# Optimization experiments

Hardware: AMD Instinct MI355X
Metric: run time of the kernel (lower is better)

Reference implementation:

```python
import jax, jax.numpy as jnp
import numpy as np

B, L, HID = 2, 2048, 4096
NH, NKV, HD = 16, 4, 64
BLOCK = 16
THETA = 8000000.0
EPS = 1e-6
NEG = jnp.finfo(jnp.float32).min


def _rope_tables(theta, L, hd):
    inv_freq = 1.0 / (theta ** (np.arange(0, hd, 2, dtype=np.float32) / hd))  # [hd/2]
    t = np.arange(L, dtype=np.float32)
    freqs = np.outer(t, inv_freq)                      # [L, hd/2]
    emb = np.concatenate([freqs, freqs], axis=-1)      # [L, hd]
    return jnp.asarray(np.cos(emb)), jnp.asarray(np.sin(emb))


def setup_inputs() -> dict:
    key = jax.random.key(0)
    k1, k2, k3 = jax.random.split(key, 3)
    hidden_states = jax.random.normal(k1, (B, L, HID), dtype=jnp.float32)
    Wqkv = jax.random.normal(k2, (HID, (NH + 2 * NKV) * HD), dtype=jnp.float32) * 0.006
    Wo = jax.random.normal(k3, (NH * HD, HID), dtype=jnp.float32) * 0.006
    q_norm_w = jnp.ones((HD,), dtype=jnp.float32)
    k_norm_w = jnp.ones((HD,), dtype=jnp.float32)
    # block-diagonal causal additive mask [1,1,L,L]
    idx = jnp.arange(L)
    same_block = (idx[:, None] // BLOCK) == (idx[None, :] // BLOCK)
    causal = idx[:, None] >= idx[None, :]
    attention_mask = jnp.where(same_block & causal, 0.0, NEG)[None, None].astype(jnp.float32)
    cos1, sin1 = _rope_tables(THETA, L, HD)
    cos = jnp.broadcast_to(cos1[None], (B, L, HD))
    sin = jnp.broadcast_to(sin1[None], (B, L, HD))
    return {"hidden_states": hidden_states, "attention_mask": attention_mask,
            "cos": cos, "sin": sin, "Wqkv": Wqkv, "Wo": Wo,
            "q_norm_w": q_norm_w, "k_norm_w": k_norm_w}


def _rms_norm(x, w):
    xf = x.astype(jnp.float32)
    var = jnp.mean(xf * xf, axis=-1, keepdims=True)
    return (xf * jax.lax.rsqrt(var + EPS)).astype(x.dtype) * w


def _rotate_half(x):
    x1, x2 = jnp.split(x, 2, axis=-1)
    return jnp.concatenate([-x2, x1], axis=-1)


def reference(hidden_states, attention_mask, cos, sin, Wqkv, Wo, q_norm_w, k_norm_w):
    Bc, Lc, _ = hidden_states.shape
    qkv = hidden_states @ Wqkv                                # [B,L,(NH+2NKV)*HD]
    qkv = qkv.reshape(Bc, Lc, NH + 2 * NKV, HD)
    q, k, v = jnp.split(qkv, [NH, NH + NKV], axis=2)
    q = q.transpose(0, 2, 1, 3)                               # [B,NH,L,HD]
    k = k.transpose(0, 2, 1, 3)                               # [B,NKV,L,HD]
    v = v.transpose(0, 2, 1, 3)
    q = _rms_norm(q, q_norm_w)
    k = _rms_norm(k, k_norm_w)
    c = cos[:, None]                                          # [B,1,L,HD]
    s = sin[:, None]
    q = q * c + _rotate_half(q) * s
    k = k * c + _rotate_half(k) * s
    groups = NH // NKV
    k = jnp.repeat(k, groups, axis=1)                         # [B,NH,L,HD]
    v = jnp.repeat(v, groups, axis=1)
    scale = 1.0 / jnp.sqrt(jnp.float32(HD))
    scores = jnp.einsum('bhqd,bhkd->bhqk', q, k) * scale + attention_mask
    probs = jax.nn.softmax(scores, axis=-1)
    out = jnp.einsum('bhqk,bhkd->bhqd', probs, v)             # [B,NH,L,HD]
    out = out.transpose(0, 2, 1, 3).reshape(Bc, Lc, NH * HD)
    return out @ Wo
```

## Files before the change

### kernel.cpp

```cpp
#include <hip/hip_runtime.h>
#include <hip/hip_bf16.h>
#include <cstdint>

#define B_SZ   2
#define L_SEQ  2048
#define HID    4096
#define NH     16
#define NKV    4
#define HD     64
#define NQKV   (NH + 2*NKV)
#define QKV_N  (NQKV*HD)
#define O_N    (NH*HD)
#define M_ROWS (B_SZ*L_SEQ)
#define EPSV   1e-6f

typedef __bf16  bf16x8_t  __attribute__((ext_vector_type(8)));
typedef float   f32x4_t   __attribute__((ext_vector_type(4)));
typedef unsigned short ushort8_t __attribute__((ext_vector_type(8)));

__device__ __forceinline__ unsigned short f2b(float f) {
    union { float f; uint32_t u; } v; v.f = f;
    uint32_t r = v.u + 0x7FFFu + ((v.u >> 16) & 1u);
    return (unsigned short)(r >> 16);
}
__device__ __forceinline__ float b2f(unsigned short u) {
    union { uint32_t u; float f; } v; v.u = ((uint32_t)u) << 16;
    return v.f;
}

__device__ __forceinline__ void gload_lds16(const void* g, void* l) {
    __builtin_amdgcn_global_load_lds(
        (__attribute__((address_space(1))) void*)(g),
        (__attribute__((address_space(3))) void*)(l),
        16, 0, 0);
}

#define BARF() do { asm volatile("" ::: "memory"); \
                    __builtin_amdgcn_s_barrier();  \
                    asm volatile("" ::: "memory"); } while (0)

template <int N> __device__ __forceinline__ void vmcnt_wait() {
    if constexpr (N == 4)       asm volatile("s_waitcnt vmcnt(4)"  ::: "memory");
    else if constexpr (N == 5)  asm volatile("s_waitcnt vmcnt(5)"  ::: "memory");
    else if constexpr (N == 6)  asm volatile("s_waitcnt vmcnt(6)"  ::: "memory");
    else if constexpr (N == 8)  asm volatile("s_waitcnt vmcnt(8)"  ::: "memory");
    else if constexpr (N == 10) asm volatile("s_waitcnt vmcnt(10)" ::: "memory");
    else if constexpr (N == 12) asm volatile("s_waitcnt vmcnt(12)" ::: "memory");
    else                        asm volatile("s_waitcnt vmcnt(0)"  ::: "memory");
}

__global__ __launch_bounds__(256) void cvt_f32_bf16(const float* __restrict__ in,
                                                    unsigned short* __restrict__ out,
                                                    int n8) {
    int i = blockIdx.x * 256 + threadIdx.x;
    if (i >= n8) return;
    const float4* p = (const float4*)(in + (size_t)i * 8);
    float4 a = p[0], b = p[1];
    ushort8_t o;
    o[0]=f2b(a.x); o[1]=f2b(a.y); o[2]=f2b(a.z); o[3]=f2b(a.w);
    o[4]=f2b(b.x); o[5]=f2b(b.y); o[6]=f2b(b.z); o[7]=f2b(b.w);
    *(ushort8_t*)(out + (size_t)i * 8) = o;
}

__global__ __launch_bounds__(256) void transpose_f32_bf16(const float* __restrict__ in,
                                                          unsigned short* __restrict__ out,
                                                          int R, int C) {
    __shared__ float t[32][33];
    const int c0 = blockIdx.x * 32;
    const int r0 = blockIdx.y * 32;
    const int tx = threadIdx.x & 31;
    const int ty = threadIdx.x >> 5;
    #pragma unroll
    for (int i = 0; i < 32; i += 8)
        t[ty + i][tx] = in[(size_t)(r0 + ty + i) * C + c0 + tx];
    __syncthreads();
    #pragma unroll
    for (int i = 0; i < 32; i += 8)
        out[(size_t)(c0 + ty + i) * R + r0 + tx] = f2b(t[tx][ty + i]);
}

template <int BM, int BN, int BK, int NBUF, int NWM, int NWN, bool BURST,
          bool OBF16, typename OutT>
__global__ __launch_bounds__(512, 2)
void gemm_sb(const unsigned short* __restrict__ A,
             const unsigned short* __restrict__ Bt,
             OutT* __restrict__ C, int M, int N, int K) {
    constexpr int WM    = BM / NWM;
    constexpr int WN    = BN / NWN;
    constexpr int AF    = WM / 16;
    constexpr int BF    = WN / 16;
    constexpr int KK    = BK / 32;
    constexpr int BUF   = (BM + BN) * BK;
    constexpr int ROWS  = 4096 / BK;
    constexpr int AR    = BM / ROWS;
    constexpr int BR    = BN / ROWS;
    constexpr int RNDS  = AR + BR;
    constexpr int DEPTH = NBUF - 2;

    __shared__ unsigned short smem[NBUF * BUF];

    const int tid  = threadIdx.x;
    const int lane = tid & 63;
    const int wave = tid >> 6;
    const int wm   = wave / NWN;
    const int wn   = wave % NWN;
    const int fr   = lane & 15;
    const int fq   = lane >> 4;

    const int nbx = N / BN;
    int bid = blockIdx.x;
    const int cpx = gridDim.x >> 3;
    bid = (bid & 7) * cpx + (bid >> 3);
    const int bx = bid % nbx, by = bid / nbx;
    const int m0 = by * BM, n0 = bx * BN;

    const int srow = tid / (BK / 8);
    const int sch  = tid & (BK / 8 - 1);
    const int ssw  = (BK == 64) ? (srow & 7) : ((srow >> 1) & 3);
    const int scs  = (sch ^ ssw) << 3;
    const unsigned short* gA = A  + (size_t)(m0 + srow) * K + scs;
    const unsigned short* gB = Bt + (size_t)(n0 + srow) * K + scs;

    const int frsw = (BK == 64) ? (fr & 7) : ((fr >> 1) & 3);

    f32x4_t acc[AF][BF];
    #pragma unroll
    for (int m = 0; m < AF; m++)
        #pragma unroll
        for (int n = 0; n < BF; n++)
            acc[m][n] = (f32x4_t){0.f, 0.f, 0.f, 0.f};

    const int NT = K / BK;

    auto STAGE = [&](int T) {
        const int pb = (T % NBUF) * BUF;
        #pragma unroll
        for (int q = 0; q < AR; ++q)
            gload_lds16(gA + (size_t)(q * ROWS) * K + (size_t)T * BK,
                        &smem[pb + q * 4096 + tid * 8]);
        #pragma unroll
        for (int q = 0; q < BR; ++q)
            gload_lds16(gB + (size_t)(q * ROWS) * K + (size_t)T * BK,
                        &smem[pb + BM * BK + q * 4096 + tid * 8]);
    };

    #pragma unroll
    for (int pt = 0; pt < NBUF - 1; ++pt) STAGE(pt);
    vmcnt_wait<DEPTH * RNDS>();

    for (int t = 0; t < NT; ++t) {
        const int sb = (t % NBUF) * BUF;
        BARF();

        if constexpr (BURST) {
            bf16x8_t aF[KK][AF], bF[KK][BF];
            #pragma unroll
            for (int kk = 0; kk < KK; ++kk) {
                const int cxk = (((kk * 4 + fq) ^ frsw)) << 3;
                #pragma unroll
                for (int mm = 0; mm < AF; ++mm)
                    aF[kk][mm] = *(const bf16x8_t*)&smem[sb + (wm*WM + mm*16 + fr)*BK + cxk];
                #pragma unroll
                for (int nn = 0; nn < BF; ++nn)
                    bF[kk][nn] = *(const bf16x8_t*)&smem[sb + BM*BK + (wn*WN + nn*16 + fr)*BK + cxk];
            }
            if (t + NBUF - 1 < NT) STAGE(t + NBUF - 1);
            #pragma unroll
            for (int kk = 0; kk < KK; ++kk) {
                __builtin_amdgcn_s_setprio(1);
                #pragma unroll
                for (int mm = 0; mm < AF; ++mm)
                    #pragma unroll
                    for (int nn = 0; nn < BF; ++nn)
                        acc[mm][nn] = __builtin_amdgcn_mfma_f32_16x16x32_bf16(
                            aF[kk][mm], bF[kk][nn], acc[mm][nn], 0, 0, 0);
                __builtin_amdgcn_s_setprio(0);
            }
        } else {
            #pragma unroll
            for (int kk = 0; kk < KK; ++kk) {
                const int cxk = (((kk * 4 + fq) ^ frsw)) << 3;
                bf16x8_t aF[AF], bF[BF];
                #pragma unroll
                for (int mm = 0; mm < AF; ++mm)
                    aF[mm] = *(const bf16x8_t*)&smem[sb + (wm*WM + mm*16 + fr)*BK + cxk];
                #pragma unroll
                for (int nn = 0; nn < BF; ++nn)
                    bF[nn] = *(const bf16x8_t*)&smem[sb + BM*BK + (wn*WN + nn*16 + fr)*BK + cxk];

                if (kk == 0 && t + NBUF - 1 < NT) STAGE(t + NBUF - 1);

                __builtin_amdgcn_s_setprio(1);
                #pragma unroll
                for (int mm = 0; mm < AF; ++mm)
                    #pragma unroll
                    for (int nn = 0; nn < BF; ++nn)
                        acc[mm][nn] = __builtin_amdgcn_mfma_f32_16x16x32_bf16(
                            aF[mm], bF[nn], acc[mm][nn], 0, 0, 0);
                __builtin_amdgcn_s_setprio(0);
            }
        }

        if constexpr (DEPTH == 2) {
            if (t + 3 < NT)      { vmcnt_wait<2 * RNDS>(); }
            else if (t + 2 < NT) { vmcnt_wait<RNDS>(); }
            else if (t + 1 < NT) { vmcnt_wait<0>(); }
        } else {
            if (t + 2 < NT)      { vmcnt_wait<RNDS>(); }
            else if (t + 1 < NT) { vmcnt_wait<0>(); }
        }
    }

    const int crow = m0 + wm * WM + fq * 4;
    const int ccol = n0 + wn * WN + fr;
    #pragma unroll
    for (int m = 0; m < AF; m++)
        #pragma unroll
        for (int n = 0; n < BF; n++)
            #pragma unroll
            for (int rr = 0; rr < 4; rr++) {
                const size_t idx = (size_t)(crow + m*16 + rr) * N + ccol + n*16;
                if constexpr (OBF16) C[idx] = (OutT)f2b(acc[m][n][rr]);
                else                 C[idx] = (OutT)acc[m][n][rr];
            }
}

__global__ __launch_bounds__(64) void attn_fused(const unsigned short* __restrict__ qkv,
                                                 const float* __restrict__ cosb,
                                                 const float* __restrict__ sinb,
                                                 const float* __restrict__ qw,
                                                 const float* __restrict__ kw,
                                                 unsigned short* __restrict__ out) {
    const int h    = blockIdx.x & (NH - 1);
    const int blk  = (blockIdx.x >> 4) & 127;
    const int b    = blockIdx.x >> 11;
    const int pos0 = blk * 16;
    const int kvh  = h >> 2;

    const int lane = threadIdx.x;
    const int r    = lane >> 2;
    const int qp   = lane & 3;
    const int d0   = qp * 16;

    __shared__ float qs[16][65];
    __shared__ float ks[16][65];
    __shared__ float vs[16][65];
    __shared__ float ps[16][17];

    const size_t rowb = ((size_t)(b * L_SEQ + pos0 + r)) * NQKV;
    const unsigned short* qptr = qkv + (rowb + h) * HD + d0;
    const unsigned short* kptr = qkv + (rowb + NH + kvh) * HD + d0;
    const unsigned short* vptr = qkv + (rowb + NH + NKV + kvh) * HD + d0;
    const size_t csrow = ((size_t)(b * L_SEQ + pos0 + r)) * HD + d0;

    float q[16], k[16], v[16], cs[16], sn[16];
    {
        ushort8_t q0 = *(const ushort8_t*)&qptr[0], q1 = *(const ushort8_t*)&qptr[8];
        ushort8_t k0 = *(const ushort8_t*)&kptr[0], k1 = *(const ushort8_t*)&kptr[8];
        ushort8_t v0 = *(const ushort8_t*)&vptr[0], v1 = *(const ushort8_t*)&vptr[8];
        #pragma unroll
        for (int i = 0; i < 8; i++) {
            q[i] = b2f(q0[i]); q[i+8] = b2f(q1[i]);
            k[i] = b2f(k0[i]); k[i+8] = b2f(k1[i]);
            v[i] = b2f(v0[i]); v[i+8] = b2f(v1[i]);
        }
        #pragma unroll
        for (int i = 0; i < 16; i += 4) {
            *(float4*)&cs[i] = *(const float4*)&cosb[csrow + i];
            *(float4*)&sn[i] = *(const float4*)&sinb[csrow + i];
        }
    }

    float sq = 0.f, sk = 0.f;
    #pragma unroll
    for (int i = 0; i < 16; i++) { sq += q[i]*q[i]; sk += k[i]*k[i]; }
    sq += __shfl_xor(sq, 1); sq += __shfl_xor(sq, 2);
    sk += __shfl_xor(sk, 1); sk += __shfl_xor(sk, 2);
    const float rq = rsqrtf(sq * (1.f / HD) + EPSV);
    const float rk = rsqrtf(sk * (1.f / HD) + EPSV);

    const float sgn = (qp < 2) ? -1.f : 1.f;
    #pragma unroll
    for (int i = 0; i < 16; i++) {
        float qn = q[i] * rq * qw[d0 + i];
        float kn = k[i] * rk * kw[d0 + i];
        float qo = __shfl_xor(qn, 2);
        float ko = __shfl_xor(kn, 2);
        qs[r][d0 + i] = qn * cs[i] + sgn * qo * sn[i];
        ks[r][d0 + i] = kn * cs[i] + sgn * ko * sn[i];
        vs[r][d0 + i] = v[i];
    }
    __syncthreads();

    float sc[4] = {0.f, 0.f, 0.f, 0.f};
    for (int d = 0; d < 64; d++) {
        const float qd = qs[r][d];
        sc[0] += qd * ks[qp     ][d];
        sc[1] += qd * ks[qp +  4][d];
        sc[2] += qd * ks[qp +  8][d];
        sc[3] += qd * ks[qp + 12][d];
    }
    #pragma unroll
    for (int cc = 0; cc < 4; cc++) {
        const int c = qp + cc * 4;
        sc[cc] = (c <= r) ? sc[cc] * 0.125f : -3.0e38f;
    }
    float mx = fmaxf(fmaxf(sc[0], sc[1]), fmaxf(sc[2], sc[3]));
    mx = fmaxf(mx, __shfl_xor(mx, 1));
    mx = fmaxf(mx, __shfl_xor(mx, 2));
    float e[4], sum = 0.f;
    #pragma unroll
    for (int cc = 0; cc < 4; cc++) { e[cc] = __expf(sc[cc] - mx); sum += e[cc]; }
    sum += __shfl_xor(sum, 1); sum += __shfl_xor(sum, 2);
    const float inv = 1.f / sum;
    #pragma unroll
    for (int cc = 0; cc < 4; cc++) ps[r][qp + cc * 4] = e[cc] * inv;
    __syncthreads();

    float o[16];
    #pragma unroll
    for (int i = 0; i < 16; i++) o[i] = 0.f;
    #pragma unroll
    for (int c = 0; c < 16; c++) {
        const float p = ps[r][c];
        #pragma unroll
        for (int i = 0; i < 16; i++) o[i] += p * vs[c][d0 + i];
    }

    __attribute__((aligned(16))) unsigned short ob[16];
    #pragma unroll
    for (int i = 0; i < 16; i++) ob[i] = f2b(o[i]);
    unsigned short* optr = out + (((size_t)(b * L_SEQ + pos0 + r) * NH + h) * HD) + d0;
    *(uint4*)optr       = *(uint4*)&ob[0];
    *((uint4*)optr + 1) = *(uint4*)&ob[8];
}

extern "C" void kernel_launch(void* const* d_in, const int* in_sizes, int n_in,
                              void* d_out, int out_size, void* d_ws, size_t ws_size,
                              hipStream_t stream) {
    const float* hid  = (const float*)d_in[0];
    const float* cosb = (const float*)d_in[2];
    const float* sinb = (const float*)d_in[3];
    const float* Wqkv = (const float*)d_in[4];
    const float* Wo   = (const float*)d_in[5];
    const float* qw   = (const float*)d_in[6];
    const float* kw   = (const float*)d_in[7];
    float* outp = (float*)d_out;

    char* ws = (char*)d_ws;
    unsigned short* Hb    = (unsigned short*)ws; ws += (size_t)M_ROWS * HID * 2;
    unsigned short* WqkvT = (unsigned short*)ws; ws += (size_t)QKV_N * HID * 2;
    unsigned short* WoT   = (unsigned short*)ws; ws += (size_t)HID * O_N * 2;
    unsigned short* qkvb  = (unsigned short*)ws; ws += (size_t)M_ROWS * QKV_N * 2;
    unsigned short* attnb = (unsigned short*)ws;

    {
        int n8 = (M_ROWS * HID) / 8;
        cvt_f32_bf16<<<(n8 + 255) / 256, 256, 0, stream>>>(hid, Hb, n8);
    }
    transpose_f32_bf16<<<dim3(QKV_N / 32, HID / 32), 256, 0, stream>>>(Wqkv, WqkvT, HID, QKV_N);
    transpose_f32_bf16<<<dim3(HID / 32, O_N / 32),  256, 0, stream>>>(Wo,   WoT,   O_N, HID);

    gemm_sb<128, 192, 64, 3, 2, 4, false, true, unsigned short>
        <<<dim3((M_ROWS / 128) * (QKV_N / 192)), 512, 0, stream>>>
        (Hb, WqkvT, qkvb, M_ROWS, QKV_N, HID);

    attn_fused<<<dim3(B_SZ * (L_SEQ / 16) * NH), 64, 0, stream>>>(qkvb, cosb, sinb, qw, kw, attnb);

    gemm_sb<256, 128, 64, 3, 4, 2, true, false, float>
        <<<dim3((M_ROWS / 256) * (HID / 128)), 512, 0, stream>>>
        (attnb, WoT, outp, M_ROWS, HID, O_N);
}
```

Baseline: 151.9 us.

## Fuse hidden-state bf16 conversion into QKV GEMM and merge weight transposes

The QKV projection GEMM now reads fp32 hidden states directly. It converts them to bf16 in registers and writes them into swizzled LDS, with the global loads prefetched two tiles ahead. This removes the separate conversion kernel and its bf16 round trip through memory. The two weight transposes are merged into a single launch, and the output GEMM switches to 256x256 tiles with BK=32 and 4 buffers. The BURST variant is dropped. In exchange, the A-tile writes are synchronous register-to-LDS stores, and the larger output tile launches fewer blocks.

```diff
diff --git a/kernel.cpp b/kernel.cpp
--- a/kernel.cpp
+++ b/kernel.cpp
@@ -38,36 +38,37 @@
 #define BARF() do { asm volatile("" ::: "memory"); \
                     __builtin_amdgcn_s_barrier();  \
                     asm volatile("" ::: "memory"); } while (0)
+#define FENCE() asm volatile("" ::: "memory")
+#define LGKM0() asm volatile("s_waitcnt lgkmcnt(0)" ::: "memory")
 
 template <int N> __device__ __forceinline__ void vmcnt_wait() {
-    if constexpr (N == 4)       asm volatile("s_waitcnt vmcnt(4)"  ::: "memory");
+    if constexpr (N == 3)       asm volatile("s_waitcnt vmcnt(3)"  ::: "memory");
+    else if constexpr (N == 4)  asm volatile("s_waitcnt vmcnt(4)"  ::: "memory");
     else if constexpr (N == 5)  asm volatile("s_waitcnt vmcnt(5)"  ::: "memory");
     else if constexpr (N == 6)  asm volatile("s_waitcnt vmcnt(6)"  ::: "memory");
     else if constexpr (N == 8)  asm volatile("s_waitcnt vmcnt(8)"  ::: "memory");
-    else if constexpr (N == 10) asm volatile("s_waitcnt vmcnt(10)" ::: "memory");
     else if constexpr (N == 12) asm volatile("s_waitcnt vmcnt(12)" ::: "memory");
     else                        asm volatile("s_waitcnt vmcnt(0)"  ::: "memory");
 }
 
-__global__ __launch_bounds__(256) void cvt_f32_bf16(const float* __restrict__ in,
-                                                    unsigned short* __restrict__ out,
-                                                    int n8) {
-    int i = blockIdx.x * 256 + threadIdx.x;
-    if (i >= n8) return;
-    const float4* p = (const float4*)(in + (size_t)i * 8);
-    float4 a = p[0], b = p[1];
-    ushort8_t o;
-    o[0]=f2b(a.x); o[1]=f2b(a.y); o[2]=f2b(a.z); o[3]=f2b(a.w);
-    o[4]=f2b(b.x); o[5]=f2b(b.y); o[6]=f2b(b.z); o[7]=f2b(b.w);
-    *(ushort8_t*)(out + (size_t)i * 8) = o;
-}
-
-__global__ __launch_bounds__(256) void transpose_f32_bf16(const float* __restrict__ in,
-                                                          unsigned short* __restrict__ out,
-                                                          int R, int C) {
+__global__ __launch_bounds__(256) void transpose_both(const float* __restrict__ Wqkv,
+                                                      unsigned short* __restrict__ WqkvT,
+                                                      const float* __restrict__ Wo,
+                                                      unsigned short* __restrict__ WoT) {
     __shared__ float t[32][33];
-    const int c0 = blockIdx.x * 32;
-    const int r0 = blockIdx.y * 32;
+    const float* in;
+    unsigned short* out;
+    int R, C, bx, by;
+    if (blockIdx.x < 6144) {
+        in = Wqkv; out = WqkvT; R = HID; C = QKV_N;
+        bx = blockIdx.x % 48; by = blockIdx.x / 48;
+    } else {
+        int b = blockIdx.x - 6144;
+        in = Wo; out = WoT; R = O_N; C = HID;
+        bx = b % 128; by = b / 128;
+    }
+    const int c0 = bx * 32;
+    const int r0 = by * 32;
     const int tx = threadIdx.x & 31;
     const int ty = threadIdx.x >> 5;
     #pragma unroll
@@ -79,8 +80,142 @@
         out[(size_t)(c0 + ty + i) * R + r0 + tx] = f2b(t[tx][ty + i]);
 }
 
-template <int BM, int BN, int BK, int NBUF, int NWM, int NWN, bool BURST,
-          bool OBF16, typename OutT>
+#define G1_BM   128
+#define G1_BN   192
+#define G1_BUF  ((G1_BM + G1_BN) * 64)
+#define G1_NT   (HID / 64)
+
+__global__ __launch_bounds__(512, 2)
+void gemm1_f32a(const float* __restrict__ A32,
+                const unsigned short* __restrict__ Bt,
+                unsigned short* __restrict__ C) {
+    constexpr int AF = 4, BF = 3;
+    __shared__ unsigned short smem[3 * G1_BUF];
+
+    const int tid  = threadIdx.x;
+    const int lane = tid & 63;
+    const int wave = tid >> 6;
+    const int wm   = wave >> 2;
+    const int wn   = wave & 3;
+    const int fr   = lane & 15;
+    const int fq   = lane >> 4;
+
+    const int nbx = QKV_N / G1_BN;
+    int bid = blockIdx.x;
+    const int cpx = gridDim.x >> 3;
+    bid = (bid & 7) * cpx + (bid >> 3);
+    const int bx = bid % nbx, by = bid / nbx;
+    const int m0 = by * G1_BM, n0 = bx * G1_BN;
+
+    const int srowA = tid >> 3;
+    const int ca    = tid & 7;
+    const float* gAf = A32 + (size_t)(m0 + srowA) * HID + ca * 8;
+    const int   wAsh = (ca ^ (srowA & 7)) << 3;
+
+    const int srow = tid >> 3;
+    const int scs  = ((tid & 7) ^ (srow & 7)) << 3;
+    const unsigned short* gB = Bt + (size_t)(n0 + srow) * HID + scs;
+
+    const int frsw = fr & 7;
+
+    f32x4_t acc[AF][BF];
+    #pragma unroll
+    for (int m = 0; m < AF; m++)
+        #pragma unroll
+        for (int n = 0; n < BF; n++)
+            acc[m][n] = (f32x4_t){0.f, 0.f, 0.f, 0.f};
+
+    auto LOAD_A = [&](int T, float4 av[2][2]) {
+        const float* g = gAf + (size_t)T * 64;
+        #pragma unroll
+        for (int q = 0; q < 2; ++q) {
+            av[q][0] = *(const float4*)(g + (size_t)q * 64 * HID);
+            av[q][1] = *(const float4*)(g + (size_t)q * 64 * HID + 4);
+        }
+    };
+    auto WRITE_A = [&](int T, float4 av[2][2]) {
+        const int pb = (T % 3) * G1_BUF;
+        #pragma unroll
+        for (int q = 0; q < 2; ++q) {
+            ushort8_t o;
+            o[0] = f2b(av[q][0].x); o[1] = f2b(av[q][0].y);
+            o[2] = f2b(av[q][0].z); o[3] = f2b(av[q][0].w);
+            o[4] = f2b(av[q][1].x); o[5] = f2b(av[q][1].y);
+            o[6] = f2b(av[q][1].z); o[7] = f2b(av[q][1].w);
+            *(ushort8_t*)&smem[pb + (q * 64 + srowA) * 64 + wAsh] = o;
+        }
+    };
+    auto STAGE_B = [&](int T) {
+        const int pb = (T % 3) * G1_BUF;
+        #pragma unroll
+        for (int q = 0; q < 3; ++q)
+            gload_lds16(gB + (size_t)(q * 64) * HID + (size_t)T * 64,
+                        &smem[pb + G1_BM * 64 + q * 4096 + tid * 8]);
+    };
+
+    {
+        float4 av0[2][2], av1[2][2];
+        LOAD_A(0, av0); LOAD_A(1, av1);
+        FENCE();
+        STAGE_B(0); STAGE_B(1);
+        WRITE_A(0, av0);
+        WRITE_A(1, av1);
+        vmcnt_wait<3>();
+        LGKM0();
+    }
+
+    float4 av[2][2];
+    for (int t = 0; t < G1_NT; ++t) {
+        const int sb = (t % 3) * G1_BUF;
+        BARF();
+
+        #pragma unroll
+        for (int kk = 0; kk < 2; ++kk) {
+            const int cxk = (((kk * 4 + fq) ^ frsw)) << 3;
+            bf16x8_t aF[AF], bF[BF];
+            #pragma unroll
+            for (int mm = 0; mm < AF; ++mm)
+                aF[mm] = *(const bf16x8_t*)&smem[sb + (wm*64 + mm*16 + fr)*64 + cxk];
+            #pragma unroll
+            for (int nn = 0; nn < BF; ++nn)
+                bF[nn] = *(const bf16x8_t*)&smem[sb + G1_BM*64 + (wn*48 + nn*16 + fr)*64 + cxk];
+
+            if (kk == 0 && t + 2 < G1_NT) {
+                LOAD_A(t + 2, av);
+                FENCE();
+                STAGE_B(t + 2);
+            }
+
+            __builtin_amdgcn_s_setprio(1);
+            #pragma unroll
+            for (int mm = 0; mm < AF; ++mm)
+                #pragma unroll
+                for (int nn = 0; nn < BF; ++nn)
+                    acc[mm][nn] = __builtin_amdgcn_mfma_f32_16x16x32_bf16(
+                        aF[mm], bF[nn], acc[mm][nn], 0, 0, 0);
+            __builtin_amdgcn_s_setprio(0);
+        }
+
+        if (t + 2 < G1_NT) {
+            WRITE_A(t + 2, av);
+        } else if (t + 1 < G1_NT) {
+            vmcnt_wait<0>();
+        }
+        LGKM0();
+    }
+
+    const int crow = m0 + wm * 64 + fq * 4;
+    const int ccol = n0 + wn * 48 + fr;
+    #pragma unroll
+    for (int m = 0; m < AF; m++)
+        #pragma unroll
+        for (int n = 0; n < BF; n++)
+            #pragma unroll
+            for (int rr = 0; rr < 4; rr++)
+                C[(size_t)(crow + m*16 + rr) * QKV_N + ccol + n*16] = f2b(acc[m][n][rr]);
+}
+
+template <int BM, int BN, int BK, int NBUF, int NWM, int NWN, bool OBF16, typename OutT>
 __global__ __launch_bounds__(512, 2)
 void gemm_sb(const unsigned short* __restrict__ A,
              const unsigned short* __restrict__ Bt,
@@ -152,53 +287,27 @@
         const int sb = (t % NBUF) * BUF;
         BARF();
 
-        if constexpr (BURST) {
-            bf16x8_t aF[KK][AF], bF[KK][BF];
-            #pragma unroll
-            for (int kk = 0; kk < KK; ++kk) {
-                const int cxk = (((kk * 4 + fq) ^ frsw)) << 3;
-                #pragma unroll
-                for (int mm = 0; mm < AF; ++mm)
-                    aF[kk][mm] = *(const bf16x8_t*)&smem[sb + (wm*WM + mm*16 + fr)*BK + cxk];
+        #pragma unroll
+        for (int kk = 0; kk < KK; ++kk) {
+            const int cxk = (((kk * 4 + fq) ^ frsw)) << 3;
+            bf16x8_t aF[AF], bF[BF];
+            #pragma unroll
+            for (int mm = 0; mm < AF; ++mm)
+                aF[mm] = *(const bf16x8_t*)&smem[sb + (wm*WM + mm*16 + fr)*BK + cxk];
+            #pragma unroll
+            for (int nn = 0; nn < BF; ++nn)
+                bF[nn] = *(const bf16x8_t*)&smem[sb + BM*BK + (wn*WN + nn*16 + fr)*BK + cxk];
+
+            if (kk == 0 && t + NBUF - 1 < NT) STAGE(t + NBUF - 1);
+
+            __builtin_amdgcn_s_setprio(1);
+            #pragma unroll
+            for (int mm = 0; mm < AF; ++mm)
                 #pragma unroll
                 for (int nn = 0; nn < BF; ++nn)
-                    bF[kk][nn] = *(const bf16x8_t*)&smem[sb + BM*BK + (wn*WN + nn*16 + fr)*BK + cxk];
-            }
-            if (t + NBUF - 1 < NT) STAGE(t + NBUF - 1);
-            #pragma unroll
-            for (int kk = 0; kk < KK; ++kk) {
-                __builtin_amdgcn_s_setprio(1);
-                #pragma unroll
-                for (int mm = 0; mm < AF; ++mm)
-                    #pragma unroll
-                    for (int nn = 0; nn < BF; ++nn)
-                        acc[mm][nn] = __builtin_amdgcn_mfma_f32_16x16x32_bf16(
-                            aF[kk][mm], bF[kk][nn], acc[mm][nn], 0, 0, 0);
-                __builtin_amdgcn_s_setprio(0);
-            }
-        } else {
-            #pragma unroll
-            for (int kk = 0; kk < KK; ++kk) {
-                const int cxk = (((kk * 4 + fq) ^ frsw)) << 3;
-                bf16x8_t aF[AF], bF[BF];
-                #pragma unroll
-                for (int mm = 0; mm < AF; ++mm)
-                    aF[mm] = *(const bf16x8_t*)&smem[sb + (wm*WM + mm*16 + fr)*BK + cxk];
-                #pragma unroll
-                for (int nn = 0; nn < BF; ++nn)
-                    bF[nn] = *(const bf16x8_t*)&smem[sb + BM*BK + (wn*WN + nn*16 + fr)*BK + cxk];
-
-                if (kk == 0 && t + NBUF - 1 < NT) STAGE(t + NBUF - 1);
-
-                __builtin_amdgcn_s_setprio(1);
-                #pragma unroll
-                for (int mm = 0; mm < AF; ++mm)
-                    #pragma unroll
-                    for (int nn = 0; nn < BF; ++nn)
-                        acc[mm][nn] = __builtin_amdgcn_mfma_f32_16x16x32_bf16(
-                            aF[mm], bF[nn], acc[mm][nn], 0, 0, 0);
-                __builtin_amdgcn_s_setprio(0);
-            }
+                    acc[mm][nn] = __builtin_amdgcn_mfma_f32_16x16x32_bf16(
+                        aF[mm], bF[nn], acc[mm][nn], 0, 0, 0);
+            __builtin_amdgcn_s_setprio(0);
         }
 
         if constexpr (DEPTH == 2) {
@@ -348,26 +457,19 @@
     float* outp = (float*)d_out;
 
     char* ws = (char*)d_ws;
-    unsigned short* Hb    = (unsigned short*)ws; ws += (size_t)M_ROWS * HID * 2;
     unsigned short* WqkvT = (unsigned short*)ws; ws += (size_t)QKV_N * HID * 2;
     unsigned short* WoT   = (unsigned short*)ws; ws += (size_t)HID * O_N * 2;
     unsigned short* qkvb  = (unsigned short*)ws; ws += (size_t)M_ROWS * QKV_N * 2;
     unsigned short* attnb = (unsigned short*)ws;
 
-    {
-        int n8 = (M_ROWS * HID) / 8;
-        cvt_f32_bf16<<<(n8 + 255) / 256, 256, 0, stream>>>(hid, Hb, n8);
-    }
-    transpose_f32_bf16<<<dim3(QKV_N / 32, HID / 32), 256, 0, stream>>>(Wqkv, WqkvT, HID, QKV_N);
-    transpose_f32_bf16<<<dim3(HID / 32, O_N / 32),  256, 0, stream>>>(Wo,   WoT,   O_N, HID);
-
-    gemm_sb<128, 192, 64, 3, 2, 4, false, true, unsigned short>
-        <<<dim3((M_ROWS / 128) * (QKV_N / 192)), 512, 0, stream>>>
-        (Hb, WqkvT, qkvb, M_ROWS, QKV_N, HID);
+    transpose_both<<<dim3(6144 + 4096), 256, 0, stream>>>(Wqkv, WqkvT, Wo, WoT);
+
+    gemm1_f32a<<<dim3((M_ROWS / 128) * (QKV_N / 192)), 512, 0, stream>>>
+        (hid, WqkvT, qkvb);
 
     attn_fused<<<dim3(B_SZ * (L_SEQ / 16) * NH), 64, 0, stream>>>(qkvb, cosb, sinb, qw, kw, attnb);
 
-    gemm_sb<256, 128, 64, 3, 4, 2, true, false, float>
-        <<<dim3((M_ROWS / 256) * (HID / 128)), 512, 0, stream>>>
+    gemm_sb<256, 256, 32, 4, 2, 4, false, float>
+        <<<dim3((M_ROWS / 256) * (HID / 256)), 512, 0, stream>>>
         (attnb, WoT, outp, M_ROWS, HID, O_N);
 }
```

New measurement: 148.1 us. -2.5%, faster.
